# Optimization experiments

Hardware: AMD Instinct MI355X
Metric: run time of the kernel (lower is better)

The kernel has to match this reference:

```python
import jax, jax.numpy as jnp
import numpy as np

# Model config (matches init_kwargs)
D_MODEL = 1536
NUM_HEADS = 16
QUERY_GROUPS = 4
HEAD_DIM = D_MODEL // NUM_HEADS  # 96
HEADS_PER_GROUP = NUM_HEADS // QUERY_GROUPS
ROPE_THETA = 10000.0
B, T, GH, GW = 2, 16, 16, 16
S = GH * GW  # spatial patches per frame
QKV_OUT = NUM_HEADS * HEAD_DIM + 2 * QUERY_GROUPS * HEAD_DIM  # 2304


def setup_inputs() -> dict:
    key = jax.random.key(0)
    k1, k2, k3 = jax.random.split(key, 3)
    x = jax.random.normal(k1, (B, T, S, D_MODEL), dtype=jnp.float32)
    padding_mask = jnp.ones((B * T, S), dtype=jnp.int32)
    # nn.Linear weights stored as [out, in]; y = x @ W.T
    w_qkv = jax.random.normal(k2, (QKV_OUT, D_MODEL), dtype=jnp.float32) * (1.0 / np.sqrt(D_MODEL))
    w_o = jax.random.normal(k3, (D_MODEL, D_MODEL), dtype=jnp.float32) * (1.0 / np.sqrt(D_MODEL))
    return {"x": x, "padding_mask": padding_mask, "w_qkv": w_qkv, "w_o": w_o}


def _rot_half(seg, cos, sin):
    # seg: [..., d]; half-split rotary rotation
    d = seg.shape[-1] // 2
    x1, x2 = seg[..., :d], seg[..., d:]
    return jnp.concatenate([x1 * cos - x2 * sin, x1 * sin + x2 * cos], axis=-1)


def _cos_sin(pos, seg_dim):
    # pos: [L] -> cos/sin [L, seg_dim//2]
    inv_freq = 1.0 / (ROPE_THETA ** (jnp.arange(seg_dim // 2, dtype=jnp.float32) * 2.0 / seg_dim))
    ang = pos.astype(jnp.float32)[:, None] * inv_freq[None, :]
    return jnp.cos(ang), jnp.sin(ang)


def _apply_rope3d(x):
    # x: [B*T, S, heads, HEAD_DIM]; head_dim split equally over (t, h, w) axes
    seg = HEAD_DIM // 3  # 32
    t_pos = jnp.tile(jnp.arange(T), B)            # [B*T] temporal index per attention-batch row
    h_pos = jnp.repeat(jnp.arange(GH), GW)        # [S]
    w_pos = jnp.tile(jnp.arange(GW), GH)          # [S]
    ct, st = _cos_sin(t_pos, seg)  # [B*T, seg/2]
    ch, sh = _cos_sin(h_pos, seg)  # [S, seg/2]
    cw, sw = _cos_sin(w_pos, seg)
    xt = _rot_half(x[..., :seg], ct[:, None, None, :], st[:, None, None, :])
    xh = _rot_half(x[..., seg:2 * seg], ch[None, :, None, :], sh[None, :, None, :])
    xw = _rot_half(x[..., 2 * seg:], cw[None, :, None, :], sw[None, :, None, :])
    return jnp.concatenate([xt, xh, xw], axis=-1)


def reference(x, padding_mask, w_qkv, w_o):
    # Spatial attention mode: [B, T, S, D] -> [B*T, S, D]
    xs = x.reshape(B * T, S, D_MODEL)
    qkv = jnp.einsum('bsd,od->bso', xs, w_qkv)  # [B*T, S, QKV_OUT]
    q_end = NUM_HEADS * HEAD_DIM
    k_end = q_end + QUERY_GROUPS * HEAD_DIM
    q = qkv[..., :q_end].reshape(B * T, S, NUM_HEADS, HEAD_DIM)
    k = qkv[..., q_end:k_end].reshape(B * T, S, QUERY_GROUPS, HEAD_DIM)
    v = qkv[..., k_end:].reshape(B * T, S, QUERY_GROUPS, HEAD_DIM)
    # RoPE3D on q and k
    q = _apply_rope3d(q)
    k = _apply_rope3d(k)
    # GQA: extend kv heads to num_heads (repeat_interleave)
    k = jnp.repeat(k, HEADS_PER_GROUP, axis=2)  # [B*T, S, NUM_HEADS, HEAD_DIM]
    v = jnp.repeat(v, HEADS_PER_GROUP, axis=2)
    scale = 1.0 / np.sqrt(HEAD_DIM)
    scores = jnp.einsum('bqhd,bkhd->bhqk', q, k) * scale  # [B*T, H, S, S]
    mask = (padding_mask != 0)[:, None, None, :]  # [B*T, 1, 1, S], True = attend
    scores = jnp.where(mask, scores, jnp.float32(-1e9))
    probs = jax.nn.softmax(scores, axis=-1)
    attn = jnp.einsum('bhqk,bkhd->bqhd', probs, v).reshape(B * T, S, D_MODEL)
    out = jnp.einsum('bsd,od->bso', attn, w_o)
    return out.reshape(B, T, S, D_MODEL)
```

## Files before the change

kernel.cpp:

```cpp
#include <hip/hip_runtime.h>
#include <hip/hip_bf16.h>
#include <stdint.h>

typedef __attribute__((ext_vector_type(8))) short short8;
typedef __attribute__((ext_vector_type(4))) float f32x4;
typedef __attribute__((ext_vector_type(4))) float f4;
typedef __attribute__((ext_vector_type(4))) short s4;

typedef __attribute__((address_space(1))) const void gvoid_t;
typedef __attribute__((address_space(3))) void lvoid_t;

__device__ __forceinline__ void gload_lds16(const void* g, void* l) {
  __builtin_amdgcn_global_load_lds((gvoid_t*)g, (lvoid_t*)l, 16, 0, 0);
}

__device__ __forceinline__ ushort f2b(float f) {
  union { float f; uint32_t u; } v; v.f = f;
  return (ushort)((v.u + 0x7fffu + ((v.u >> 16) & 1u)) >> 16);
}
__device__ __forceinline__ float b2f(ushort b) {
  union { uint32_t u; float f; } v; v.u = ((uint32_t)b) << 16;
  return v.f;
}

template <int N> __device__ __forceinline__ void wait_vmcnt();
template <> __device__ __forceinline__ void wait_vmcnt<0>() { asm volatile("s_waitcnt vmcnt(0)" ::: "memory"); }
template <> __device__ __forceinline__ void wait_vmcnt<1>() { asm volatile("s_waitcnt vmcnt(1)" ::: "memory"); }
template <> __device__ __forceinline__ void wait_vmcnt<2>() { asm volatile("s_waitcnt vmcnt(2)" ::: "memory"); }
template <> __device__ __forceinline__ void wait_vmcnt<3>() { asm volatile("s_waitcnt vmcnt(3)" ::: "memory"); }

__device__ __forceinline__ void wait_lgkm0() {
  asm volatile("s_waitcnt lgkmcnt(0)" ::: "memory");
  __builtin_amdgcn_sched_barrier(0);
}

template <int ROWS>
__device__ __forceinline__ void stage_rows(const ushort* __restrict__ g, int ldg,
                                           ushort* lds, int w, int l, int sc) {
#pragma unroll
  for (int i = 0; i < ROWS / 64; ++i)
    gload_lds16(g + (size_t)(i * 64 + w * 8 + (l >> 3)) * ldg + sc * 8,
                lds + i * 4096 + w * 512);
  if constexpr ((ROWS % 64) != 0) {
    if (w < (ROWS % 64) / 8)
      gload_lds16(g + (size_t)((ROWS / 64) * 64 + w * 8 + (l >> 3)) * ldg + sc * 8,
                  lds + (ROWS / 64) * 4096 + w * 512);
  }
}

__global__ void cvt_kernel(const float* __restrict__ in, ushort* __restrict__ out, int n4) {
  int i = blockIdx.x * 256 + threadIdx.x;
  if (i < n4) {
    f4 v = ((const f4*)in)[i];
    s4 o;
    o.x = (short)f2b(v.x); o.y = (short)f2b(v.y);
    o.z = (short)f2b(v.z); o.w = (short)f2b(v.w);
    ((s4*)out)[i] = o;
  }
}

template <int BN, typename OutT>
__global__ __launch_bounds__(512, 2) void gemm3(const ushort* __restrict__ A,
                                                const ushort* __restrict__ B,
                                                OutT* __restrict__ C,
                                                int N, int K) {
  constexpr int NF = BN / 32;
  constexpr int NH0 = (NF + 1) / 2;
  constexpr int NH1 = NF - NH0;
  constexpr int RB = BN / 2;
  constexpr int B0FULL = RB / 64;
  constexpr int B0EXTRA = (RB % 64) / 8;

  __shared__ ushort As[2][256 * 64];
  __shared__ ushort Bs[2][BN * 64];

  const int tid = threadIdx.x;
  const int l = tid & 63, w = tid >> 6;
  const int wr = w >> 1, wc = w & 1;
  const int r16 = l & 15, kh = l >> 4;
  const int sc = (l & 7) ^ (l >> 3);

  const int xcd = blockIdx.x & 7;
  const int ii = blockIdx.x >> 3;
  const int bm = xcd * 4 + (ii & 3);
  const int bn = ii >> 2;
  const ushort* Ag = A + (size_t)bm * 256 * K;
  const ushort* Bg = B + (size_t)bn * BN * K;
  const int NT = K >> 6;

  stage_rows<128>(Ag,                   K, &As[0][0],        w, l, sc);
  stage_rows<128>(Ag + (size_t)128 * K, K, &As[0][128 * 64], w, l, sc);
  stage_rows<RB >(Bg,                   K, &Bs[0][0],        w, l, sc);
  stage_rows<RB >(Bg + (size_t)RB * K,  K, &Bs[0][RB * 64],  w, l, sc);
  stage_rows<RB >(Bg + 64,              K, &Bs[1][0],        w, l, sc);
  if (B0EXTRA > 0 && w < B0EXTRA) wait_vmcnt<B0FULL + 1>(); else wait_vmcnt<B0FULL>();
  __builtin_amdgcn_s_barrier();

  f32x4 acc[4][NF] = {};
  short8 afr[4][2], bfr[NH0][2];

  for (int u = 0; u < NT; ++u) {
    const int cur = u & 1;
    const ushort* Asb = &As[cur][0];
    const ushort* Bsb = &Bs[cur][0];
    ushort* Asn = &As[cur ^ 1][0];
    ushort* Bsn = &Bs[cur ^ 1][0];
    const int kt1 = (u + 1) << 6, kt2 = (u + 2) << 6;
    const bool st1 = (u + 1 < NT), st2 = (u + 2 < NT);

#pragma unroll
    for (int n = 0; n < NH0; ++n)
#pragma unroll
      for (int ks = 0; ks < 2; ++ks)
        bfr[n][ks] = *(const short8*)(Bsb + (wc * RB + n * 16 + r16) * 64 +
                                      (((ks * 4 + kh) ^ (r16 & 7)) * 8));
#pragma unroll
    for (int mm = 0; mm < 4; ++mm)
#pragma unroll
      for (int ks = 0; ks < 2; ++ks)
        afr[mm][ks] = *(const short8*)(Asb + (wr * 64 + mm * 16 + r16) * 64 +
                                       (((ks * 4 + kh) ^ (r16 & 7)) * 8));
    if (st1) {
      stage_rows<128>(Ag + kt1,                    K, Asn,            w, l, sc);
      stage_rows<128>(Ag + (size_t)128 * K + kt1,  K, Asn + 128 * 64, w, l, sc);
      stage_rows<RB >(Bg + (size_t)RB * K + kt1,   K, Bsn + RB * 64,  w, l, sc);
    }
    wait_lgkm0();
    __builtin_amdgcn_s_setprio(1);
#pragma unroll
    for (int mm = 0; mm < 4; ++mm)
#pragma unroll
      for (int n = 0; n < NH0; ++n)
#pragma unroll
        for (int ks = 0; ks < 2; ++ks)
          acc[mm][n] = __builtin_amdgcn_mfma_f32_16x16x32_bf16(afr[mm][ks], bfr[n][ks], acc[mm][n], 0, 0, 0);
    __builtin_amdgcn_s_setprio(0);

#pragma unroll
    for (int n = 0; n < NH1; ++n)
#pragma unroll
      for (int ks = 0; ks < 2; ++ks)
        bfr[n][ks] = *(const short8*)(Bsb + (wc * RB + (NH0 + n) * 16 + r16) * 64 +
                                      (((ks * 4 + kh) ^ (r16 & 7)) * 8));
    wait_lgkm0();
    __builtin_amdgcn_s_setprio(1);
#pragma unroll
    for (int mm = 0; mm < 4; ++mm)
#pragma unroll
      for (int n = 0; n < NH1; ++n)
#pragma unroll
        for (int ks = 0; ks < 2; ++ks)
          acc[mm][NH0 + n] = __builtin_amdgcn_mfma_f32_16x16x32_bf16(afr[mm][ks], bfr[n][ks], acc[mm][NH0 + n], 0, 0, 0);
    __builtin_amdgcn_s_setprio(0);

    __builtin_amdgcn_s_barrier();
    if (st2) stage_rows<RB>(Bg + kt2, K, &Bs[cur][0], w, l, sc);
    if (st2) { if (B0EXTRA > 0 && w < B0EXTRA) wait_vmcnt<B0FULL + 1>(); else wait_vmcnt<B0FULL>(); }
    else wait_vmcnt<0>();
    __builtin_amdgcn_s_barrier();
  }

  const int rowb = bm * 256 + wr * 64;
  const int colb = bn * BN + wc * RB;
#pragma unroll
  for (int m = 0; m < 4; ++m)
#pragma unroll
    for (int n = 0; n < NF; ++n)
#pragma unroll
      for (int r = 0; r < 4; ++r) {
        int row = rowb + m * 16 + kh * 4 + r;
        int col = colb + n * 16 + r16;
        float val = acc[m][n][r];
        if constexpr (sizeof(OutT) == 2) C[(size_t)row * N + col] = f2b(val);
        else                             C[(size_t)row * N + col] = val;
      }
}

__global__ void rope_kernel(const ushort* __restrict__ qkv,
                            ushort* __restrict__ Qo, ushort* __restrict__ Ko,
                            ushort* __restrict__ Vt) {
  const int UNITS = 1344;
  int idx = blockIdx.x * 256 + threadIdx.x;
  if (idx >= 8192 * UNITS) return;
  int row = idx / UNITS;
  int unit = idx - row * UNITS;
  int bt = row >> 8, s = row & 255;
  const ushort* qr = qkv + (size_t)row * 2304;
  if (unit < 960) {
    int head, p;
    size_t srcoff;
    ushort* dst;
    if (unit < 768) {
      head = unit / 48; p = unit % 48;
      srcoff = (size_t)head * 96;
      dst = Qo + ((size_t)(bt * 16 + head) * 256 + s) * 96;
    } else {
      int u = unit - 768;
      head = u / 48; p = u % 48;
      srcoff = 1536 + (size_t)head * 96;
      dst = Ko + ((size_t)(bt * 4 + head) * 256 + s) * 96;
    }
    int seg = p >> 4, i = p & 15;
    int pos = (seg == 0) ? (bt & 15) : ((seg == 1) ? (s >> 4) : (s & 15));
    float inv_freq = __expf(-(float)i * 0.5756462732485115f);
    float ang = (float)pos * inv_freq;
    float sn, c;
    __sincosf(ang, &sn, &c);
    float x1 = b2f(qr[srcoff + seg * 32 + i]);
    float x2 = b2f(qr[srcoff + seg * 32 + i + 16]);
    dst[seg * 32 + i]      = f2b(x1 * c - x2 * sn);
    dst[seg * 32 + i + 16] = f2b(x1 * sn + x2 * c);
  } else {
    int u = unit - 960;
    int g = u / 96, d = u - g * 96;
    Vt[((size_t)(bt * 4 + g) * 96 + d) * 256 + s] = qr[1920 + (size_t)g * 96 + d];
  }
}

__global__ __launch_bounds__(512, 2) void attn2_kernel(
    const ushort* __restrict__ Q,
    const ushort* __restrict__ Kr,
    const ushort* __restrict__ Vt,
    const int* __restrict__ mask,
    ushort* __restrict__ Out) {
  __shared__ ushort Ks[256 * 104];
  __shared__ ushort Vs[96 * 264];
  __shared__ ushort Ps[8][16 * 136];
  __shared__ float Mb[256];

  const int b = blockIdx.x;
  const int qt = b & 1;
  const int g = (b >> 1) & 3;
  const int bt = b >> 3;
  const int t = threadIdx.x;
  const int l = t & 63, w = t >> 6;
  const int r16 = l & 15, kh = l >> 4;
  const int h = g * 4 + (w >> 1);
  const int qc = w & 1;

  const ushort* Kp = Kr + (size_t)(bt * 4 + g) * 256 * 96;
  const ushort* Vp = Vt + (size_t)(bt * 4 + g) * 96 * 256;

  {
    int r = t >> 1, ch = t & 1;
#pragma unroll
    for (int j = 0; j < 6; ++j)
      *(short8*)(&Ks[r * 104 + ch * 48 + j * 8]) =
          *(const short8*)(Kp + (size_t)r * 96 + ch * 48 + j * 8);
  }
#pragma unroll
  for (int i = 0; i < 6; ++i) {
    int c = t + i * 512;
    int vr = c >> 5, vc = c & 31;
    *(short8*)(&Vs[vr * 264 + vc * 8]) =
        *(const short8*)(Vp + (size_t)vr * 256 + vc * 8);
  }
  if (t < 256) Mb[t] = mask[bt * 256 + t] ? 0.0f : -1.0e9f;
  __syncthreads();

  const ushort* Qp = Q + ((size_t)(bt * 16 + h) * 256 + qt * 128 + qc * 64) * 96;
  ushort* Pw = &Ps[w][0];
  const float scale = 0.10206207261596575f;

#pragma unroll
  for (int mp = 0; mp < 2; ++mp) {
    const int qb = mp * 32;

    short8 qfA[3], qfB[3];
#pragma unroll
    for (int kc = 0; kc < 3; ++kc) {
      qfA[kc] = *(const short8*)(Qp + (size_t)(qb + r16) * 96 + kc * 32 + kh * 8);
      qfB[kc] = *(const short8*)(Qp + (size_t)(qb + 16 + r16) * 96 + kc * 32 + kh * 8);
    }

    f32x4 scA[16] = {}, scB[16] = {};
#pragma unroll
    for (int f = 0; f < 16; ++f) {
#pragma unroll
      for (int kc = 0; kc < 3; ++kc) {
        short8 kf = *(const short8*)(&Ks[(f * 16 + r16) * 104 + kc * 32 + kh * 8]);
        scA[f] = __builtin_amdgcn_mfma_f32_16x16x32_bf16(qfA[kc], kf, scA[f], 0, 0, 0);
        scB[f] = __builtin_amdgcn_mfma_f32_16x16x32_bf16(qfB[kc], kf, scB[f], 0, 0, 0);
      }
    }

#pragma unroll
    for (int f = 0; f < 16; ++f) {
      float mb = Mb[f * 16 + r16];
#pragma unroll
      for (int r = 0; r < 4; ++r) {
        scA[f][r] = scA[f][r] * scale + mb;
        scB[f][r] = scB[f][r] * scale + mb;
      }
    }

    float invA[4], invB[4];
#pragma unroll
    for (int reg = 0; reg < 4; ++reg) {
      float mxA = -3.0e38f, mxB = -3.0e38f;
#pragma unroll
      for (int f = 0; f < 16; ++f) { mxA = fmaxf(mxA, scA[f][reg]); mxB = fmaxf(mxB, scB[f][reg]); }
      for (int o = 8; o >= 1; o >>= 1) { mxA = fmaxf(mxA, __shfl_xor(mxA, o, 64)); mxB = fmaxf(mxB, __shfl_xor(mxB, o, 64)); }
      float smA = 0.f, smB = 0.f;
#pragma unroll
      for (int f = 0; f < 16; ++f) {
        float pA = __expf(scA[f][reg] - mxA);
        float pB = __expf(scB[f][reg] - mxB);
        scA[f][reg] = pA; scB[f][reg] = pB;
        smA += pA; smB += pB;
      }
      for (int o = 8; o >= 1; o >>= 1) { smA += __shfl_xor(smA, o, 64); smB += __shfl_xor(smB, o, 64); }
      invA[reg] = 1.0f / smA;
      invB[reg] = 1.0f / smB;
    }

    short8 pfA[8], pfB[8];
#pragma unroll
    for (int ck = 0; ck < 2; ++ck) {
#pragma unroll
      for (int f = 0; f < 8; ++f)
#pragma unroll
        for (int reg = 0; reg < 4; ++reg)
          Pw[(kh * 4 + reg) * 136 + f * 16 + r16] = f2b(scA[ck * 8 + f][reg]);
#pragma unroll
      for (int kc = 0; kc < 4; ++kc)
        pfA[ck * 4 + kc] = *(const short8*)(&Pw[r16 * 136 + kc * 32 + kh * 8]);
    }
#pragma unroll
    for (int ck = 0; ck < 2; ++ck) {
#pragma unroll
      for (int f = 0; f < 8; ++f)
#pragma unroll
        for (int reg = 0; reg < 4; ++reg)
          Pw[(kh * 4 + reg) * 136 + f * 16 + r16] = f2b(scB[ck * 8 + f][reg]);
#pragma unroll
      for (int kc = 0; kc < 4; ++kc)
        pfB[ck * 4 + kc] = *(const short8*)(&Pw[r16 * 136 + kc * 32 + kh * 8]);
    }

    f32x4 oA[6] = {}, oB[6] = {};
#pragma unroll
    for (int dt = 0; dt < 6; ++dt) {
#pragma unroll
      for (int kc = 0; kc < 8; ++kc) {
        short8 vf = *(const short8*)(&Vs[(dt * 16 + r16) * 264 + kc * 32 + kh * 8]);
        oA[dt] = __builtin_amdgcn_mfma_f32_16x16x32_bf16(pfA[kc], vf, oA[dt], 0, 0, 0);
        oB[dt] = __builtin_amdgcn_mfma_f32_16x16x32_bf16(pfB[kc], vf, oB[dt], 0, 0, 0);
      }
    }

    const int rbase = bt * 256 + qt * 128 + qc * 64 + qb;
#pragma unroll
    for (int dt = 0; dt < 6; ++dt)
#pragma unroll
      for (int reg = 0; reg < 4; ++reg) {
        int col = h * 96 + dt * 16 + r16;
        Out[(size_t)(rbase + kh * 4 + reg) * 1536 + col]      = f2b(oA[dt][reg] * invA[reg]);
        Out[(size_t)(rbase + 16 + kh * 4 + reg) * 1536 + col] = f2b(oB[dt][reg] * invB[reg]);
      }
  }
}

extern "C" void kernel_launch(void* const* d_in, const int* in_sizes, int n_in,
                              void* d_out, int out_size, void* d_ws, size_t ws_size,
                              hipStream_t stream) {
  const float* x     = (const float*)d_in[0];
  const int* pmask   = (const int*)d_in[1];
  const float* w_qkv = (const float*)d_in[2];
  const float* w_o   = (const float*)d_in[3];
  float* out = (float*)d_out;

  char* ws = (char*)d_ws;
  ushort* Xb  = (ushort*)(ws + 0);
  ushort* Wq  = (ushort*)(ws + 25165824);
  ushort* Wo  = (ushort*)(ws + 32243712);
  ushort* QKV = (ushort*)(ws + 36962304);
  ushort* Qr  = (ushort*)(ws + 74711040);
  ushort* Kr  = (ushort*)(ws + 99876864);
  ushort* Vt  = (ushort*)(ws + 106168320);
  ushort* Attn = Xb;

  cvt_kernel<<<3145728 / 256, 256, 0, stream>>>(x, Xb, 3145728);
  cvt_kernel<<<884736 / 256, 256, 0, stream>>>(w_qkv, Wq, 884736);
  cvt_kernel<<<589824 / 256, 256, 0, stream>>>(w_o, Wo, 589824);

  gemm3<288, ushort><<<256, 512, 0, stream>>>(Xb, Wq, QKV, 2304, 1536);

  rope_kernel<<<(8192 * 1344) / 256, 256, 0, stream>>>(QKV, Qr, Kr, Vt);

  attn2_kernel<<<256, 512, 0, stream>>>(Qr, Kr, Vt, pmask, Attn);

  gemm3<192, float><<<256, 512, 0, stream>>>(Attn, Wo, out, 1536, 1536);
}
```

Before: 175.8 us.

## Shrink GEMM tiles to 128-row, K=32 blocks with more CTAs; precompute RoPE table

After: 191.3 us. 8.8% more time.

```diff
diff --git a/kernel.cpp b/kernel.cpp
--- a/kernel.cpp
+++ b/kernel.cpp
@@ -25,27 +25,10 @@
 
 template <int N> __device__ __forceinline__ void wait_vmcnt();
 template <> __device__ __forceinline__ void wait_vmcnt<0>() { asm volatile("s_waitcnt vmcnt(0)" ::: "memory"); }
-template <> __device__ __forceinline__ void wait_vmcnt<1>() { asm volatile("s_waitcnt vmcnt(1)" ::: "memory"); }
-template <> __device__ __forceinline__ void wait_vmcnt<2>() { asm volatile("s_waitcnt vmcnt(2)" ::: "memory"); }
-template <> __device__ __forceinline__ void wait_vmcnt<3>() { asm volatile("s_waitcnt vmcnt(3)" ::: "memory"); }
 
 __device__ __forceinline__ void wait_lgkm0() {
   asm volatile("s_waitcnt lgkmcnt(0)" ::: "memory");
   __builtin_amdgcn_sched_barrier(0);
-}
-
-template <int ROWS>
-__device__ __forceinline__ void stage_rows(const ushort* __restrict__ g, int ldg,
-                                           ushort* lds, int w, int l, int sc) {
-#pragma unroll
-  for (int i = 0; i < ROWS / 64; ++i)
-    gload_lds16(g + (size_t)(i * 64 + w * 8 + (l >> 3)) * ldg + sc * 8,
-                lds + i * 4096 + w * 512);
-  if constexpr ((ROWS % 64) != 0) {
-    if (w < (ROWS % 64) / 8)
-      gload_lds16(g + (size_t)((ROWS / 64) * 64 + w * 8 + (l >> 3)) * ldg + sc * 8,
-                  lds + (ROWS / 64) * 4096 + w * 512);
-  }
 }
 
 __global__ void cvt_kernel(const float* __restrict__ in, ushort* __restrict__ out, int n4) {
@@ -60,108 +43,81 @@
 }
 
 template <int BN, typename OutT>
-__global__ __launch_bounds__(512, 2) void gemm3(const ushort* __restrict__ A,
+__global__ __launch_bounds__(256, 3) void gemm4(const ushort* __restrict__ A,
                                                 const ushort* __restrict__ B,
                                                 OutT* __restrict__ C,
                                                 int N, int K) {
   constexpr int NF = BN / 32;
-  constexpr int NH0 = (NF + 1) / 2;
-  constexpr int NH1 = NF - NH0;
-  constexpr int RB = BN / 2;
-  constexpr int B0FULL = RB / 64;
-  constexpr int B0EXTRA = (RB % 64) / 8;
-
-  __shared__ ushort As[2][256 * 64];
-  __shared__ ushort Bs[2][BN * 64];
+  constexpr int HB = BN / 2;
+  constexpr int BI = BN / 64;
+
+  __shared__ ushort As[2][128 * 32];
+  __shared__ ushort Bs[2][BN * 32];
 
   const int tid = threadIdx.x;
   const int l = tid & 63, w = tid >> 6;
   const int wr = w >> 1, wc = w & 1;
   const int r16 = l & 15, kh = l >> 4;
-  const int sc = (l & 7) ^ (l >> 3);
+  const int kc = (l & 3) ^ ((l >> 3) & 3);
+  const int srow = w * 16 + (l >> 2);
+  const int ksw = (r16 >> 1) & 3;
 
   const int xcd = blockIdx.x & 7;
   const int ii = blockIdx.x >> 3;
-  const int bm = xcd * 4 + (ii & 3);
-  const int bn = ii >> 2;
-  const ushort* Ag = A + (size_t)bm * 256 * K;
+  const int bm = xcd * 8 + (ii & 7);
+  const int bn = ii >> 3;
+  const ushort* Ag = A + (size_t)bm * 128 * K;
   const ushort* Bg = B + (size_t)bn * BN * K;
-  const int NT = K >> 6;
-
-  stage_rows<128>(Ag,                   K, &As[0][0],        w, l, sc);
-  stage_rows<128>(Ag + (size_t)128 * K, K, &As[0][128 * 64], w, l, sc);
-  stage_rows<RB >(Bg,                   K, &Bs[0][0],        w, l, sc);
-  stage_rows<RB >(Bg + (size_t)RB * K,  K, &Bs[0][RB * 64],  w, l, sc);
-  stage_rows<RB >(Bg + 64,              K, &Bs[1][0],        w, l, sc);
-  if (B0EXTRA > 0 && w < B0EXTRA) wait_vmcnt<B0FULL + 1>(); else wait_vmcnt<B0FULL>();
+  const int NT = K >> 5;
+
+#pragma unroll
+  for (int i = 0; i < 2; ++i)
+    gload_lds16(Ag + (size_t)(i * 64 + srow) * K + kc * 8, &As[0][i * 2048 + w * 512]);
+#pragma unroll
+  for (int i = 0; i < BI; ++i)
+    gload_lds16(Bg + (size_t)(i * 64 + srow) * K + kc * 8, &Bs[0][i * 2048 + w * 512]);
+  wait_vmcnt<0>();
   __builtin_amdgcn_s_barrier();
 
   f32x4 acc[4][NF] = {};
-  short8 afr[4][2], bfr[NH0][2];
 
   for (int u = 0; u < NT; ++u) {
     const int cur = u & 1;
-    const ushort* Asb = &As[cur][0];
-    const ushort* Bsb = &Bs[cur][0];
-    ushort* Asn = &As[cur ^ 1][0];
-    ushort* Bsn = &Bs[cur ^ 1][0];
-    const int kt1 = (u + 1) << 6, kt2 = (u + 2) << 6;
-    const bool st1 = (u + 1 < NT), st2 = (u + 2 < NT);
-
-#pragma unroll
-    for (int n = 0; n < NH0; ++n)
-#pragma unroll
-      for (int ks = 0; ks < 2; ++ks)
-        bfr[n][ks] = *(const short8*)(Bsb + (wc * RB + n * 16 + r16) * 64 +
-                                      (((ks * 4 + kh) ^ (r16 & 7)) * 8));
-#pragma unroll
-    for (int mm = 0; mm < 4; ++mm)
-#pragma unroll
-      for (int ks = 0; ks < 2; ++ks)
-        afr[mm][ks] = *(const short8*)(Asb + (wr * 64 + mm * 16 + r16) * 64 +
-                                       (((ks * 4 + kh) ^ (r16 & 7)) * 8));
-    if (st1) {
-      stage_rows<128>(Ag + kt1,                    K, Asn,            w, l, sc);
-      stage_rows<128>(Ag + (size_t)128 * K + kt1,  K, Asn + 128 * 64, w, l, sc);
-      stage_rows<RB >(Bg + (size_t)RB * K + kt1,   K, Bsn + RB * 64,  w, l, sc);
-    }
+    short8 afr[4], bfr[NF];
+#pragma unroll
+    for (int m = 0; m < 4; ++m)
+      afr[m] = *(const short8*)(&As[cur][(wr * 64 + m * 16 + r16) * 32 + ((kh ^ ksw) * 8)]);
+#pragma unroll
+    for (int n = 0; n < NF; ++n)
+      bfr[n] = *(const short8*)(&Bs[cur][(wc * HB + n * 16 + r16) * 32 + ((kh ^ ksw) * 8)]);
+
+    if (u + 1 < NT) {
+      const int ko = (u + 1) * 32;
+#pragma unroll
+      for (int i = 0; i < 2; ++i)
+        gload_lds16(Ag + (size_t)(i * 64 + srow) * K + ko + kc * 8, &As[cur ^ 1][i * 2048 + w * 512]);
+#pragma unroll
+      for (int i = 0; i < BI; ++i)
+        gload_lds16(Bg + (size_t)(i * 64 + srow) * K + ko + kc * 8, &Bs[cur ^ 1][i * 2048 + w * 512]);
+    }
+
     wait_lgkm0();
     __builtin_amdgcn_s_setprio(1);
 #pragma unroll
-    for (int mm = 0; mm < 4; ++mm)
-#pragma unroll
-      for (int n = 0; n < NH0; ++n)
-#pragma unroll
-        for (int ks = 0; ks < 2; ++ks)
-          acc[mm][n] = __builtin_amdgcn_mfma_f32_16x16x32_bf16(afr[mm][ks], bfr[n][ks], acc[mm][n], 0, 0, 0);
+    for (int m = 0; m < 4; ++m)
+#pragma unroll
+      for (int n = 0; n < NF; ++n)
+        acc[m][n] = __builtin_amdgcn_mfma_f32_16x16x32_bf16(afr[m], bfr[n], acc[m][n], 0, 0, 0);
     __builtin_amdgcn_s_setprio(0);
 
-#pragma unroll
-    for (int n = 0; n < NH1; ++n)
-#pragma unroll
-      for (int ks = 0; ks < 2; ++ks)
-        bfr[n][ks] = *(const short8*)(Bsb + (wc * RB + (NH0 + n) * 16 + r16) * 64 +
-                                      (((ks * 4 + kh) ^ (r16 & 7)) * 8));
-    wait_lgkm0();
-    __builtin_amdgcn_s_setprio(1);
-#pragma unroll
-    for (int mm = 0; mm < 4; ++mm)
-#pragma unroll
-      for (int n = 0; n < NH1; ++n)
-#pragma unroll
-        for (int ks = 0; ks < 2; ++ks)
-          acc[mm][NH0 + n] = __builtin_amdgcn_mfma_f32_16x16x32_bf16(afr[mm][ks], bfr[n][ks], acc[mm][NH0 + n], 0, 0, 0);
-    __builtin_amdgcn_s_setprio(0);
-
-    __builtin_amdgcn_s_barrier();
-    if (st2) stage_rows<RB>(Bg + kt2, K, &Bs[cur][0], w, l, sc);
-    if (st2) { if (B0EXTRA > 0 && w < B0EXTRA) wait_vmcnt<B0FULL + 1>(); else wait_vmcnt<B0FULL>(); }
-    else wait_vmcnt<0>();
-    __builtin_amdgcn_s_barrier();
-  }
-
-  const int rowb = bm * 256 + wr * 64;
-  const int colb = bn * BN + wc * RB;
+    if (u + 1 < NT) {
+      wait_vmcnt<0>();
+      __builtin_amdgcn_s_barrier();
+    }
+  }
+
+  const int rowb = bm * 128 + wr * 64;
+  const int colb = bn * BN + wc * HB;
 #pragma unroll
   for (int m = 0; m < 4; ++m)
 #pragma unroll
@@ -176,7 +132,18 @@
       }
 }
 
+__global__ void rope_tab_kernel(float2* __restrict__ tab) {
+  int t = threadIdx.x;
+  int pos = t >> 4, i = t & 15;
+  float inv_freq = __expf(-(float)i * 0.5756462732485115f);
+  float ang = (float)pos * inv_freq;
+  float sn, c;
+  __sincosf(ang, &sn, &c);
+  tab[t] = make_float2(c, sn);
+}
+
 __global__ void rope_kernel(const ushort* __restrict__ qkv,
+                            const float2* __restrict__ tab,
                             ushort* __restrict__ Qo, ushort* __restrict__ Ko,
                             ushort* __restrict__ Vt) {
   const int UNITS = 1344;
@@ -202,10 +169,8 @@
     }
     int seg = p >> 4, i = p & 15;
     int pos = (seg == 0) ? (bt & 15) : ((seg == 1) ? (s >> 4) : (s & 15));
-    float inv_freq = __expf(-(float)i * 0.5756462732485115f);
-    float ang = (float)pos * inv_freq;
-    float sn, c;
-    __sincosf(ang, &sn, &c);
+    float2 cs = tab[pos * 16 + i];
+    float c = cs.x, sn = cs.y;
     float x1 = b2f(qr[srcoff + seg * 32 + i]);
     float x2 = b2f(qr[srcoff + seg * 32 + i + 16]);
     dst[seg * 32 + i]      = f2b(x1 * c - x2 * sn);
@@ -378,17 +343,19 @@
   ushort* Qr  = (ushort*)(ws + 74711040);
   ushort* Kr  = (ushort*)(ws + 99876864);
   ushort* Vt  = (ushort*)(ws + 106168320);
+  float2* Tab = (float2*)(ws + 112459776);
   ushort* Attn = Xb;
 
   cvt_kernel<<<3145728 / 256, 256, 0, stream>>>(x, Xb, 3145728);
   cvt_kernel<<<884736 / 256, 256, 0, stream>>>(w_qkv, Wq, 884736);
   cvt_kernel<<<589824 / 256, 256, 0, stream>>>(w_o, Wo, 589824);
-
-  gemm3<288, ushort><<<256, 512, 0, stream>>>(Xb, Wq, QKV, 2304, 1536);
-
-  rope_kernel<<<(8192 * 1344) / 256, 256, 0, stream>>>(QKV, Qr, Kr, Vt);
+  rope_tab_kernel<<<1, 256, 0, stream>>>(Tab);
+
+  gemm4<192, ushort><<<768, 256, 0, stream>>>(Xb, Wq, QKV, 2304, 1536);
+
+  rope_kernel<<<(8192 * 1344) / 256, 256, 0, stream>>>(QKV, Tab, Qr, Kr, Vt);
 
   attn2_kernel<<<256, 512, 0, stream>>>(Qr, Kr, Vt, pmask, Attn);
 
-  gemm3<192, float><<<256, 512, 0, stream>>>(Attn, Wo, out, 1536, 1536);
-}
+  gemm4<128, float><<<768, 256, 0, stream>>>(Attn, Wo, out, 1536, 1536);
+}
```
